# Optimization experiments

Measured on AMD Instinct MI355X. Metric: run time of the kernel, lower is better.

Reference implementation:

```python
import jax, jax.numpy as jnp
import numpy as np
from jax import lax

B, T, F = 8, 512, 128          # batch, mel time, mel freq
DM, DS, DC, EXP, NL = 384, 16, 4, 2, 12
DI = EXP * DM                   # 768 inner width
DTR = (DM + 15) // 16           # 24, mamba_ssm dt_rank='auto'
PT = PF = 16
L = (T // PT) * (F // PF)       # 256 patches
NC = 4


def setup_inputs() -> dict:
    key = jax.random.key(0)
    ks = iter(jax.random.split(key, 24))
    def n(shape, s=0.02):
        return jax.random.normal(next(ks), shape, jnp.float32) * s
    return {
        "x": jax.random.normal(next(ks), (B, T, F), jnp.float32),
        "patch_w": n((DM, PT, PF)),
        "patch_b": jnp.zeros((DM,), jnp.float32),
        "pos_embed": n((1, L, DM)),
        "ln_g": jnp.ones((NL, DM), jnp.float32),
        "ln_b": jnp.zeros((NL, DM), jnp.float32),
        "in_proj_w": n((NL, 2 * DI, DM)),
        "conv_w": n((NL, DI, DC), 0.1),
        "conv_b": jnp.zeros((NL, DI), jnp.float32),
        "x_proj_w": n((NL, DTR + 2 * DS, DI)),
        "dt_proj_w": n((NL, DI, DTR), 0.1),
        "dt_proj_b": n((NL, DI), 0.1),
        "A_log": jnp.tile(jnp.log(jnp.arange(1, DS + 1, dtype=jnp.float32))[None, None, :], (NL, DI, 1)),
        "Dskip": jnp.ones((NL, DI), jnp.float32),
        "out_proj_w": n((NL, DM, DI)),
        "fn_g": jnp.ones((DM,), jnp.float32),
        "fn_b": jnp.zeros((DM,), jnp.float32),
        "head_w": n((NC, DM)),
        "head_b": jnp.zeros((NC,), jnp.float32),
    }


def _layernorm(x, g, b):
    m = x.mean(-1, keepdims=True)
    v = jnp.var(x, axis=-1, keepdims=True)
    return (x - m) * lax.rsqrt(v + 1e-5) * g + b


def _silu(v):
    return v * jax.nn.sigmoid(v)


def _mamba_block(x, p):
    # x: [B, L, DM]; residual Mamba block (pre-LN, dropout=identity in eval)
    ln_g, ln_b, Wi, cw, cb, Wx, Wdt, bdt, A_log, Dsk, Wo = p
    res = x
    h = _layernorm(x, ln_g, ln_b)
    xz = jnp.einsum('bld,ed->ble', h, Wi)          # [B,L,2*DI]
    u, z = jnp.split(xz, 2, axis=-1)
    # causal depthwise conv1d, kernel DC (small, unrolled)
    up = jnp.pad(u, ((0, 0), (DC - 1, 0), (0, 0)))
    u = sum(up[:, k:k + L, :] * cw[:, k] for k in range(DC)) + cb
    u = _silu(u)
    proj = jnp.einsum('bld,ed->ble', u, Wx)        # [B,L,DTR+2*DS]
    dt, Bm, Cm = jnp.split(proj, [DTR, DTR + DS], axis=-1)
    delta = jax.nn.softplus(jnp.einsum('blr,dr->bld', dt, Wdt) + bdt)  # [B,L,DI]
    A = -jnp.exp(A_log)                            # [DI, DS]
    dA = jnp.exp(delta[..., None] * A)             # [B,L,DI,DS]
    dBu = (delta * u)[..., None] * Bm[:, :, None, :]

    def step(hst, inp):
        dA_t, dBu_t, C_t = inp
        hst = dA_t * hst + dBu_t                   # [B,DI,DS]
        return hst, jnp.einsum('bdn,bn->bd', hst, C_t)

    h0 = jnp.zeros((x.shape[0], DI, DS), x.dtype)
    _, ys = lax.scan(step, h0, (dA.swapaxes(0, 1), dBu.swapaxes(0, 1), Cm.swapaxes(0, 1)))
    y = ys.swapaxes(0, 1) + u * Dsk                # [B,L,DI]
    y = y * _silu(z)
    return res + jnp.einsum('bld,ed->ble', y, Wo)


def reference(x, patch_w, patch_b, pos_embed, ln_g, ln_b, in_proj_w, conv_w, conv_b,
              x_proj_w, dt_proj_w, dt_proj_b, A_log, Dskip, out_proj_w,
              fn_g, fn_b, head_w, head_b):
    Bn = x.shape[0]
    # patch embed = non-overlapping 16x16 conv == blocked reshape + einsum
    patches = x.reshape(Bn, T // PT, PT, F // PF, PF)
    tok = jnp.einsum('bhpwq,dpq->bhwd', patches, patch_w) + patch_b
    tok = tok.reshape(Bn, L, DM) + pos_embed

    def layer(carry, p):
        return _mamba_block(carry, p), None

    tok, _ = lax.scan(layer, tok, (ln_g, ln_b, in_proj_w, conv_w, conv_b,
                                   x_proj_w, dt_proj_w, dt_proj_b, A_log, Dskip, out_proj_w))
    tok = _layernorm(tok, fn_g, fn_b)
    pooled = tok.mean(axis=1)
    return pooled @ head_w.T + head_b
```

## Files before the change

kernel.cpp:

```cpp
#include <hip/hip_runtime.h>
#include <math.h>

namespace {

constexpr int kB   = 8;
constexpr int kL   = 256;
constexpr int kTok = 2048;
constexpr int kDM  = 384;
constexpr int kDI  = 768;
constexpr int kDS  = 16;
constexpr int kDTR = 24;
constexpr int kPROJ = 56;
constexpr int kNL  = 12;

constexpr int kWIN  = 2 * kDI * kDM;
constexpr int kWOUT = kDM * kDI;
constexpr int kWX   = kPROJ * kDI;
constexpr int kWTOT = kWIN + kWOUT + kWX;

typedef float f32x4 __attribute__((ext_vector_type(4)));
typedef short short8 __attribute__((ext_vector_type(8)));

__device__ __forceinline__ float softplus_f(float x) {
  return (x > 20.f) ? x : log1pf(__expf(x));
}
__device__ __forceinline__ float silu_f(float x) {
  return x / (1.f + __expf(-x));
}
__device__ __forceinline__ unsigned short f2bf(float f) {
  union { float f; unsigned u; } v; v.f = f;
  unsigned r = v.u + 0x7FFFu + ((v.u >> 16) & 1u);
  return (unsigned short)(r >> 16);
}

__global__ __launch_bounds__(256) void patch_gemm_k(
    const float* __restrict__ x, const float* __restrict__ Bw,
    const float* __restrict__ bias, const float* __restrict__ pos,
    float* __restrict__ C) {
  __shared__ float As[16][68];
  __shared__ float Bs[16][68];
  int tid = threadIdx.x;
  int bm = blockIdx.y * 64;
  int bn = blockIdx.x * 64;
  int lr = tid >> 2;
  int lk = (tid & 3) << 2;
  int tm = (tid >> 4) << 2;
  int tn = (tid & 15) << 2;
  float acc[4][4] = {};
  for (int k0 = 0; k0 < 256; k0 += 16) {
    {
      int token = bm + lr;
      int b = token >> 8, l = token & 255;
      int h = l >> 3, w = l & 7;
      int p = k0 >> 4;
      const float* ap = x + ((size_t)(b * 512) + h * 16 + p) * 128 + w * 16 + lk;
      float4 av = *(const float4*)ap;
      As[lk + 0][lr] = av.x; As[lk + 1][lr] = av.y;
      As[lk + 2][lr] = av.z; As[lk + 3][lr] = av.w;
    }
    {
      const float* bp = Bw + (size_t)(bn + lr) * 256 + k0 + lk;
      float4 bv = *(const float4*)bp;
      Bs[lk + 0][lr] = bv.x; Bs[lk + 1][lr] = bv.y;
      Bs[lk + 2][lr] = bv.z; Bs[lk + 3][lr] = bv.w;
    }
    __syncthreads();
    #pragma unroll
    for (int k = 0; k < 16; ++k) {
      float4 a = *(const float4*)&As[k][tm];
      float4 b = *(const float4*)&Bs[k][tn];
      float av[4] = {a.x, a.y, a.z, a.w};
      float bv[4] = {b.x, b.y, b.z, b.w};
      #pragma unroll
      for (int i = 0; i < 4; ++i)
        #pragma unroll
        for (int j = 0; j < 4; ++j)
          acc[i][j] = fmaf(av[i], bv[j], acc[i][j]);
    }
    __syncthreads();
  }
  #pragma unroll
  for (int i = 0; i < 4; ++i) {
    int row = bm + tm + i;
    #pragma unroll
    for (int j = 0; j < 4; ++j) {
      int col = bn + tn + j;
      C[(size_t)row * kDM + col] =
          acc[i][j] + bias[col] + pos[(size_t)(row & 255) * kDM + col];
    }
  }
}

template <bool BF16OUT>
__global__ __launch_bounds__(384) void ln_k(
    const float* __restrict__ in, void* __restrict__ outv,
    const float* __restrict__ g, const float* __restrict__ bb,
    float* __restrict__ proj_zero) {
  int t = blockIdx.x, d = threadIdx.x;
  if (proj_zero && d < kPROJ) proj_zero[(size_t)t * kPROJ + d] = 0.f;
  float v = in[(size_t)t * kDM + d];
  float s = v, s2 = v * v;
  #pragma unroll
  for (int m = 32; m >= 1; m >>= 1) {
    s  += __shfl_xor(s, m);
    s2 += __shfl_xor(s2, m);
  }
  __shared__ float ps[6], ps2[6];
  if ((d & 63) == 0) { ps[d >> 6] = s; ps2[d >> 6] = s2; }
  __syncthreads();
  float S = 0.f, S2 = 0.f;
  #pragma unroll
  for (int i = 0; i < 6; ++i) { S += ps[i]; S2 += ps2[i]; }
  float mean = S * (1.f / 384.f);
  float var  = S2 * (1.f / 384.f) - mean * mean;
  float r = rsqrtf(var + 1e-5f);
  float o = (v - mean) * r * g[d] + bb[d];
  if (BF16OUT) ((unsigned short*)outv)[(size_t)t * kDM + d] = f2bf(o);
  else ((float*)outv)[(size_t)t * kDM + d] = o;
}

__global__ __launch_bounds__(256) void convert_all_k(
    const float* __restrict__ w_in, const float* __restrict__ w_out,
    const float* __restrict__ w_x, unsigned short* __restrict__ dst) {
  int layer = blockIdx.y;
  int i4 = (blockIdx.x * 256 + threadIdx.x) * 4;
  if (i4 >= kWTOT) return;
  const float* src;
  int off;
  if (i4 < kWIN) { src = w_in + (size_t)layer * kWIN; off = i4; }
  else if (i4 < kWIN + kWOUT) { src = w_out + (size_t)layer * kWOUT; off = i4 - kWIN; }
  else { src = w_x + (size_t)layer * kWX; off = i4 - kWIN - kWOUT; }
  float4 v = *(const float4*)(src + off);
  unsigned short o[4] = {f2bf(v.x), f2bf(v.y), f2bf(v.z), f2bf(v.w)};
  *(uint2*)(dst + (size_t)layer * kWTOT + i4) = *(const uint2*)o;
}

template <int BN, int EPIL>
__global__ __launch_bounds__(256) void bgemm_k(
    const unsigned short* __restrict__ A, int lda,
    const unsigned short* __restrict__ B, int ldb,
    float* __restrict__ C, int ldc, int N, int Kc) {
  __shared__ __align__(16) unsigned short As[4][128][8];
  __shared__ __align__(16) unsigned short Bs[4][BN][8];
  int tid = threadIdx.x;
  int bm = blockIdx.y * 128;
  int bn = blockIdx.x * BN;
  int k_begin = blockIdx.z * Kc;
  int wave = tid >> 6, lane = tid & 63;
  int lm = lane & 15, lq = lane >> 4;
  int wm, wn;
  if (BN == 128) { wm = (wave >> 1) * 64; wn = (wave & 1) * 64; }
  else           { wm = wave * 32;        wn = 0; }
  constexpr int MT = (BN == 128) ? 4 : 2;
  f32x4 acc[MT][4] = {};

  for (int kt = 0; kt < Kc; kt += 32) {
    int k0 = k_begin + kt;
    int ar0 = tid & 127, aq0 = tid >> 7;
    int aq1 = aq0 + 2;
    uint4 a0 = *(const uint4*)(A + (size_t)(bm + ar0) * lda + k0 + aq0 * 8);
    uint4 a1 = *(const uint4*)(A + (size_t)(bm + ar0) * lda + k0 + aq1 * 8);
    uint4 b0, b1;
    int br0, bq0, br1 = 0, bq1 = 0;
    if (BN == 128) {
      br0 = tid & 127; bq0 = tid >> 7; br1 = br0; bq1 = bq0 + 2;
      b0 = *(const uint4*)(B + (size_t)(bn + br0) * ldb + k0 + bq0 * 8);
      b1 = *(const uint4*)(B + (size_t)(bn + br1) * ldb + k0 + bq1 * 8);
    } else {
      br0 = tid & 63; bq0 = tid >> 6;
      if (bn + br0 < N)
        b0 = *(const uint4*)(B + (size_t)(bn + br0) * ldb + k0 + bq0 * 8);
      else
        b0 = make_uint4(0u, 0u, 0u, 0u);
    }
    __syncthreads();
    *(uint4*)&As[aq0][ar0][0] = a0;
    *(uint4*)&As[aq1][ar0][0] = a1;
    *(uint4*)&Bs[bq0][br0][0] = b0;
    if (BN == 128) *(uint4*)&Bs[bq1][br1][0] = b1;
    __syncthreads();

    short8 bfrag[4];
    #pragma unroll
    for (int ni = 0; ni < 4; ++ni)
      bfrag[ni] = *(const short8*)&Bs[lq][wn + ni * 16 + lm][0];
    #pragma unroll
    for (int mi = 0; mi < MT; ++mi) {
      short8 afrag = *(const short8*)&As[lq][wm + mi * 16 + lm][0];
      #pragma unroll
      for (int ni = 0; ni < 4; ++ni)
        acc[mi][ni] = __builtin_amdgcn_mfma_f32_16x16x32_bf16(
            afrag, bfrag[ni], acc[mi][ni], 0, 0, 0);
    }
  }

  #pragma unroll
  for (int mi = 0; mi < MT; ++mi) {
    #pragma unroll
    for (int ni = 0; ni < 4; ++ni) {
      int grow = bm + wm + mi * 16 + lq * 4;
      int gcol = bn + wn + ni * 16 + lm;
      float* cp = C + (size_t)grow * ldc + gcol;
      #pragma unroll
      for (int r = 0; r < 4; ++r) {
        float v = acc[mi][ni][r];
        if (EPIL == 0) {
          cp[(size_t)r * ldc] = v;
        } else {
          if (gcol < N) atomicAdd(cp + (size_t)r * ldc, v);
        }
      }
    }
  }
}

__global__ __launch_bounds__(256) void conv_tr_k(
    const float* __restrict__ xz, const float* __restrict__ cw,
    const float* __restrict__ cb, float* __restrict__ uT,
    float* __restrict__ sgT, unsigned short* __restrict__ u_bf) {
  int b = blockIdx.y;
  int l0 = blockIdx.x * 16;
  int tid = threadIdx.x;
  #pragma unroll
  for (int ch = 0; ch < 3; ++ch) {
    int d = ch * 256 + tid;
    float w0 = cw[d * 4], w1 = cw[d * 4 + 1], w2 = cw[d * 4 + 2], w3 = cw[d * 4 + 3];
    float bias = cb[d];
    float v[19];
    #pragma unroll
    for (int j = 0; j < 19; ++j) {
      int l = l0 - 3 + j;
      v[j] = (l >= 0) ? xz[(size_t)(b * kL + l) * (2 * kDI) + d] : 0.f;
    }
    float* up = uT + ((size_t)b * kDI + d) * kL + l0;
    float* sp = sgT + ((size_t)b * kDI + d) * kL + l0;
    #pragma unroll
    for (int i = 0; i < 16; ++i) {
      float acc = bias;
      acc = fmaf(v[i], w0, acc);
      acc = fmaf(v[i + 1], w1, acc);
      acc = fmaf(v[i + 2], w2, acc);
      acc = fmaf(v[i + 3], w3, acc);
      float o = silu_f(acc);
      up[i] = o;
      u_bf[(size_t)(b * kL + l0 + i) * kDI + d] = f2bf(o);
      float zv = xz[(size_t)(b * kL + l0 + i) * (2 * kDI) + kDI + d];
      sp[i] = silu_f(zv);
    }
  }
}

__global__ __launch_bounds__(256) void scan2_k(
    const float* __restrict__ proj, const float* __restrict__ uT,
    const float* __restrict__ sgT, const float* __restrict__ dtw,
    const float* __restrict__ dtb, const float* __restrict__ A_log,
    const float* __restrict__ Dsk, float* __restrict__ yT) {
  int d = blockIdx.x;
  int b = blockIdx.y;
  int tid = threadIdx.x;
  int c = tid >> 4;
  int n = tid & 15;
  __shared__ float sd[256], su[256], sg[256], sy[256];
  __shared__ float sh_h[16][17], sh_a[16][17];
  __shared__ float swdt[24];
  size_t rbase = ((size_t)b * kDI + d) * kL;
  su[tid] = uT[rbase + tid];
  sg[tid] = sgT[rbase + tid];
  if (tid < kDTR) swdt[tid] = dtw[(size_t)d * kDTR + tid];
  float bdt = dtb[d];
  float Aval = -__expf(A_log[d * kDS + n]);
  __syncthreads();
  {
    const float* pr = proj + (size_t)(b * kL + tid) * kPROJ;
    float acc = bdt;
    #pragma unroll
    for (int r4 = 0; r4 < 6; ++r4) {
      float4 pv = *(const float4*)(pr + r4 * 4);
      acc = fmaf(pv.x, swdt[r4 * 4 + 0], acc);
      acc = fmaf(pv.y, swdt[r4 * 4 + 1], acc);
      acc = fmaf(pv.z, swdt[r4 * 4 + 2], acc);
      acc = fmaf(pv.w, swdt[r4 * 4 + 3], acc);
    }
    sd[tid] = softplus_f(acc);
  }
  __syncthreads();

  float h = 0.f, ca = 1.f;
  float h_reg[16], ca_reg[16], cv[16];
  const float* pp = proj + (size_t)(b * kL + c * 16) * kPROJ;
  #pragma unroll
  for (int i = 0; i < 16; ++i) {
    int l = c * 16 + i;
    float dl = sd[l], uv = su[l];
    float Bv = pp[i * kPROJ + kDTR + n];
    cv[i] = pp[i * kPROJ + kDTR + kDS + n];
    float a = __expf(dl * Aval);
    h = fmaf(a, h, (dl * uv) * Bv);
    ca *= a;
    h_reg[i] = h;
    ca_reg[i] = ca;
  }
  sh_h[c][n] = h;
  sh_a[c][n] = ca;
  __syncthreads();

  float h0 = 0.f;
  for (int j = 0; j < c; ++j) h0 = fmaf(sh_a[j][n], h0, sh_h[j][n]);

  float Dv = Dsk[d];
  #pragma unroll
  for (int i = 0; i < 16; ++i) {
    int l = c * 16 + i;
    float yv = fmaf(ca_reg[i], h0, h_reg[i]) * cv[i];
    yv += __shfl_xor(yv, 1);
    yv += __shfl_xor(yv, 2);
    yv += __shfl_xor(yv, 4);
    yv += __shfl_xor(yv, 8);
    if (n == 0) sy[l] = (yv + su[l] * Dv) * sg[l];
  }
  __syncthreads();
  yT[rbase + tid] = sy[tid];
}

__global__ __launch_bounds__(256) void transpose_bf_k(
    const float* __restrict__ yT, unsigned short* __restrict__ ybf) {
  int b = blockIdx.z;
  int db = blockIdx.y;
  int lb = blockIdx.x;
  __shared__ float tile[64][65];
  int tid = threadIdx.x;
  int lx = tid & 63, dq = tid >> 6;
  const float* src = yT + ((size_t)b * kDI + db * 64) * kL + lb * 64;
  #pragma unroll
  for (int i = 0; i < 16; ++i) {
    int d = dq * 16 + i;
    tile[d][lx] = src[(size_t)d * kL + lx];
  }
  __syncthreads();
  int ly = tid >> 2, dx0 = (tid & 3) * 16;
  unsigned short tmp[16];
  #pragma unroll
  for (int i = 0; i < 16; ++i) tmp[i] = f2bf(tile[dx0 + i][ly]);
  unsigned short* dst =
      ybf + (size_t)(b * kL + lb * 64 + ly) * kDI + db * 64 + dx0;
  *(uint4*)dst = *(const uint4*)tmp;
  *(uint4*)(dst + 8) = *(const uint4*)(tmp + 8);
}

__global__ __launch_bounds__(384) void pool_k(
    const float* __restrict__ h, float* __restrict__ pooled) {
  int b = blockIdx.x, d = threadIdx.x;
  float acc = 0.f;
  for (int l = 0; l < kL; ++l) acc += h[(size_t)(b * kL + l) * kDM + d];
  pooled[b * kDM + d] = acc * (1.f / 256.f);
}

__global__ __launch_bounds__(64) void head_k(
    const float* __restrict__ pooled, const float* __restrict__ hw,
    const float* __restrict__ hb, float* __restrict__ out) {
  int b = blockIdx.x >> 2, c = blockIdx.x & 3;
  int lane = threadIdx.x;
  float acc = 0.f;
  for (int dd = lane; dd < kDM; dd += 64)
    acc = fmaf(pooled[b * kDM + dd], hw[c * kDM + dd], acc);
  #pragma unroll
  for (int m = 32; m >= 1; m >>= 1) acc += __shfl_xor(acc, m);
  if (lane == 0) out[b * 4 + c] = acc + hb[c];
}

}

extern "C" void kernel_launch(void* const* d_in, const int* in_sizes, int n_in,
                              void* d_out, int out_size, void* d_ws, size_t ws_size,
                              hipStream_t stream) {
  (void)in_sizes; (void)n_in; (void)out_size; (void)ws_size;
  const float* x        = (const float*)d_in[0];
  const float* patch_w  = (const float*)d_in[1];
  const float* patch_b  = (const float*)d_in[2];
  const float* pos      = (const float*)d_in[3];
  const float* ln_g     = (const float*)d_in[4];
  const float* ln_b     = (const float*)d_in[5];
  const float* in_w     = (const float*)d_in[6];
  const float* conv_w   = (const float*)d_in[7];
  const float* conv_b   = (const float*)d_in[8];
  const float* xproj_w  = (const float*)d_in[9];
  const float* dtproj_w = (const float*)d_in[10];
  const float* dtproj_b = (const float*)d_in[11];
  const float* A_log    = (const float*)d_in[12];
  const float* Dskip    = (const float*)d_in[13];
  const float* out_w    = (const float*)d_in[14];
  const float* fn_g     = (const float*)d_in[15];
  const float* fn_b     = (const float*)d_in[16];
  const float* head_w   = (const float*)d_in[17];
  const float* head_b   = (const float*)d_in[18];
  float* out = (float*)d_out;

  float* ws = (float*)d_ws;
  float* tok    = ws; ws += kTok * kDM;
  float* xz     = ws; ws += kTok * 2 * kDI;
  float* uT     = ws; ws += kTok * kDI;
  float* sgT    = ws; ws += kTok * kDI;
  float* proj   = ws; ws += kTok * kPROJ;
  float* yT     = ws; ws += kTok * kDI;
  float* pooled = ws; ws += kB * kDM;
  unsigned short* h_bf = (unsigned short*)ws; ws += kTok * kDM / 2;
  unsigned short* y_bf = (unsigned short*)ws; ws += kTok * kDI / 2;
  unsigned short* u_bf = (unsigned short*)ws; ws += kTok * kDI / 2;
  unsigned short* w_bf = (unsigned short*)ws; ws += (size_t)kNL * kWTOT / 2;
  float* lnout = yT;

  convert_all_k<<<dim3(kWTOT / 4 / 256, kNL), 256, 0, stream>>>(
      in_w, out_w, xproj_w, w_bf);

  patch_gemm_k<<<dim3(6, 32), 256, 0, stream>>>(x, patch_w, patch_b, pos, tok);

  for (int layer = 0; layer < kNL; ++layer) {
    const unsigned short* wl = w_bf + (size_t)layer * kWTOT;
    ln_k<true><<<kTok, kDM, 0, stream>>>(tok, h_bf, ln_g + layer * kDM,
                                         ln_b + layer * kDM, proj);
    bgemm_k<128, 0><<<dim3(12, 16, 1), 256, 0, stream>>>(
        h_bf, kDM, wl, kDM, xz, 2 * kDI, 2 * kDI, kDM);
    conv_tr_k<<<dim3(16, kB), 256, 0, stream>>>(
        xz, conv_w + layer * kDI * 4, conv_b + layer * kDI, uT, sgT, u_bf);
    bgemm_k<64, 1><<<dim3(1, 16, 6), 256, 0, stream>>>(
        u_bf, kDI, wl + kWIN + kWOUT, kDI, proj, kPROJ, kPROJ, kDI / 6);
    scan2_k<<<dim3(kDI, kB), 256, 0, stream>>>(
        proj, uT, sgT, dtproj_w + (size_t)layer * kDI * kDTR,
        dtproj_b + layer * kDI, A_log + (size_t)layer * kDI * kDS,
        Dskip + layer * kDI, yT);
    transpose_bf_k<<<dim3(4, 12, kB), 256, 0, stream>>>(yT, y_bf);
    bgemm_k<128, 1><<<dim3(3, 16, 2), 256, 0, stream>>>(
        y_bf, kDI, wl + kWIN, kDI, tok, kDM, kDM, kDI / 2);
  }

  ln_k<false><<<kTok, kDM, 0, stream>>>(tok, lnout, fn_g, fn_b, nullptr);
  pool_k<<<kB, kDM, 0, stream>>>(lnout, pooled);
  head_k<<<kB * 4, 64, 0, stream>>>(pooled, head_w, head_b, out);
}
```

Measured before the change: 1.364 ms.

## Transpose proj layout for coalesced scan reads, emit bf16 scan output, raise split-K

The x_proj GEMM epilogue now atomically adds into a transposed [B, PROJ, L] buffer, so the scan kernel reads B/C coefficients as contiguous float4 vectors and dt inputs with coalesced loads instead of strided per-token rows. The scan writes its y output directly as bf16, which halves the intermediate traffic, and the transpose kernel only shuffles bits. Split-K factors for the x_proj and out_proj GEMMs are doubled to expose more blocks, at the cost of more atomic traffic. The scan output is rounded to bf16 one step earlier, but the same rounding already happened in the transpose.

```diff
diff --git a/kernel.cpp b/kernel.cpp
--- a/kernel.cpp
+++ b/kernel.cpp
@@ -198,16 +198,19 @@
   for (int mi = 0; mi < MT; ++mi) {
     #pragma unroll
     for (int ni = 0; ni < 4; ++ni) {
-      int grow = bm + wm + mi * 16 + lq * 4;
+      int grow0 = bm + wm + mi * 16 + lq * 4;
       int gcol = bn + wn + ni * 16 + lm;
-      float* cp = C + (size_t)grow * ldc + gcol;
       #pragma unroll
       for (int r = 0; r < 4; ++r) {
         float v = acc[mi][ni][r];
+        int grow = grow0 + r;
         if (EPIL == 0) {
-          cp[(size_t)r * ldc] = v;
+          C[(size_t)grow * ldc + gcol] = v;
+        } else if (EPIL == 1) {
+          if (gcol < N) atomicAdd(&C[(size_t)grow * ldc + gcol], v);
         } else {
-          if (gcol < N) atomicAdd(cp + (size_t)r * ldc, v);
+          if (gcol < N)
+            atomicAdd(&C[((size_t)(grow >> 8) * kPROJ + gcol) * kL + (grow & 255)], v);
         }
       }
     }
@@ -250,17 +253,18 @@
   }
 }
 
-__global__ __launch_bounds__(256) void scan2_k(
-    const float* __restrict__ proj, const float* __restrict__ uT,
+__global__ __launch_bounds__(256) void scan3_k(
+    const float* __restrict__ projT, const float* __restrict__ uT,
     const float* __restrict__ sgT, const float* __restrict__ dtw,
     const float* __restrict__ dtb, const float* __restrict__ A_log,
-    const float* __restrict__ Dsk, float* __restrict__ yT) {
+    const float* __restrict__ Dsk, unsigned short* __restrict__ yT) {
   int d = blockIdx.x;
   int b = blockIdx.y;
   int tid = threadIdx.x;
   int c = tid >> 4;
   int n = tid & 15;
-  __shared__ float sd[256], su[256], sg[256], sy[256];
+  __shared__ float sd[256], su[256], sg[256];
+  __shared__ unsigned short sy[256];
   __shared__ float sh_h[16][17], sh_a[16][17];
   __shared__ float swdt[24];
   size_t rbase = ((size_t)b * kDI + d) * kL;
@@ -269,33 +273,43 @@
   if (tid < kDTR) swdt[tid] = dtw[(size_t)d * kDTR + tid];
   float bdt = dtb[d];
   float Aval = -__expf(A_log[d * kDS + n]);
-  __syncthreads();
+  const float* pb = projT + (size_t)b * kPROJ * kL;
+  float4 Bv4[4], Cv4[4];
   {
-    const float* pr = proj + (size_t)(b * kL + tid) * kPROJ;
+    const float* prB = pb + (size_t)(24 + n) * kL + c * 16;
+    const float* prC = pb + (size_t)(40 + n) * kL + c * 16;
+    #pragma unroll
+    for (int q = 0; q < 4; ++q) {
+      Bv4[q] = ((const float4*)prB)[q];
+      Cv4[q] = ((const float4*)prC)[q];
+    }
+  }
+  float B_[16], C_[16];
+  #pragma unroll
+  for (int q = 0; q < 4; ++q) {
+    B_[q * 4 + 0] = Bv4[q].x; B_[q * 4 + 1] = Bv4[q].y;
+    B_[q * 4 + 2] = Bv4[q].z; B_[q * 4 + 3] = Bv4[q].w;
+    C_[q * 4 + 0] = Cv4[q].x; C_[q * 4 + 1] = Cv4[q].y;
+    C_[q * 4 + 2] = Cv4[q].z; C_[q * 4 + 3] = Cv4[q].w;
+  }
+  __syncthreads();
+  {
     float acc = bdt;
     #pragma unroll
-    for (int r4 = 0; r4 < 6; ++r4) {
-      float4 pv = *(const float4*)(pr + r4 * 4);
-      acc = fmaf(pv.x, swdt[r4 * 4 + 0], acc);
-      acc = fmaf(pv.y, swdt[r4 * 4 + 1], acc);
-      acc = fmaf(pv.z, swdt[r4 * 4 + 2], acc);
-      acc = fmaf(pv.w, swdt[r4 * 4 + 3], acc);
-    }
+    for (int r = 0; r < kDTR; ++r)
+      acc = fmaf(pb[(size_t)r * kL + tid], swdt[r], acc);
     sd[tid] = softplus_f(acc);
   }
   __syncthreads();
 
   float h = 0.f, ca = 1.f;
-  float h_reg[16], ca_reg[16], cv[16];
-  const float* pp = proj + (size_t)(b * kL + c * 16) * kPROJ;
+  float h_reg[16], ca_reg[16];
   #pragma unroll
   for (int i = 0; i < 16; ++i) {
     int l = c * 16 + i;
-    float dl = sd[l], uv = su[l];
-    float Bv = pp[i * kPROJ + kDTR + n];
-    cv[i] = pp[i * kPROJ + kDTR + kDS + n];
+    float dl = sd[l];
     float a = __expf(dl * Aval);
-    h = fmaf(a, h, (dl * uv) * Bv);
+    h = fmaf(a, h, (dl * su[l]) * B_[i]);
     ca *= a;
     h_reg[i] = h;
     ca_reg[i] = ca;
@@ -311,36 +325,38 @@
   #pragma unroll
   for (int i = 0; i < 16; ++i) {
     int l = c * 16 + i;
-    float yv = fmaf(ca_reg[i], h0, h_reg[i]) * cv[i];
+    float yv = fmaf(ca_reg[i], h0, h_reg[i]) * C_[i];
     yv += __shfl_xor(yv, 1);
     yv += __shfl_xor(yv, 2);
     yv += __shfl_xor(yv, 4);
     yv += __shfl_xor(yv, 8);
-    if (n == 0) sy[l] = (yv + su[l] * Dv) * sg[l];
+    if (n == 0) sy[l] = f2bf((yv + su[l] * Dv) * sg[l]);
   }
   __syncthreads();
   yT[rbase + tid] = sy[tid];
 }
 
 __global__ __launch_bounds__(256) void transpose_bf_k(
-    const float* __restrict__ yT, unsigned short* __restrict__ ybf) {
+    const unsigned short* __restrict__ yT, unsigned short* __restrict__ ybf) {
   int b = blockIdx.z;
   int db = blockIdx.y;
   int lb = blockIdx.x;
   __shared__ float tile[64][65];
   int tid = threadIdx.x;
   int lx = tid & 63, dq = tid >> 6;
-  const float* src = yT + ((size_t)b * kDI + db * 64) * kL + lb * 64;
+  const unsigned short* src = yT + ((size_t)b * kDI + db * 64) * kL + lb * 64;
   #pragma unroll
   for (int i = 0; i < 16; ++i) {
-    int d = dq * 16 + i;
-    tile[d][lx] = src[(size_t)d * kL + lx];
+    int dd = dq * 16 + i;
+    unsigned ui = (unsigned)src[(size_t)dd * kL + lx] << 16;
+    tile[dd][lx] = __uint_as_float(ui);
   }
   __syncthreads();
   int ly = tid >> 2, dx0 = (tid & 3) * 16;
   unsigned short tmp[16];
   #pragma unroll
-  for (int i = 0; i < 16; ++i) tmp[i] = f2bf(tile[dx0 + i][ly]);
+  for (int i = 0; i < 16; ++i)
+    tmp[i] = (unsigned short)(__float_as_uint(tile[dx0 + i][ly]) >> 16);
   unsigned short* dst =
       ybf + (size_t)(b * kL + lb * 64 + ly) * kDI + db * 64 + dx0;
   *(uint4*)dst = *(const uint4*)tmp;
@@ -400,14 +416,14 @@
   float* xz     = ws; ws += kTok * 2 * kDI;
   float* uT     = ws; ws += kTok * kDI;
   float* sgT    = ws; ws += kTok * kDI;
-  float* proj   = ws; ws += kTok * kPROJ;
-  float* yT     = ws; ws += kTok * kDI;
+  float* projT  = ws; ws += kTok * kPROJ;
   float* pooled = ws; ws += kB * kDM;
-  unsigned short* h_bf = (unsigned short*)ws; ws += kTok * kDM / 2;
-  unsigned short* y_bf = (unsigned short*)ws; ws += kTok * kDI / 2;
-  unsigned short* u_bf = (unsigned short*)ws; ws += kTok * kDI / 2;
-  unsigned short* w_bf = (unsigned short*)ws; ws += (size_t)kNL * kWTOT / 2;
-  float* lnout = yT;
+  unsigned short* yT_bf = (unsigned short*)ws; ws += kTok * kDI / 2;
+  unsigned short* h_bf  = (unsigned short*)ws; ws += kTok * kDM / 2;
+  unsigned short* y_bf  = (unsigned short*)ws; ws += kTok * kDI / 2;
+  unsigned short* u_bf  = (unsigned short*)ws; ws += kTok * kDI / 2;
+  unsigned short* w_bf  = (unsigned short*)ws; ws += (size_t)kNL * kWTOT / 2;
+  float* lnout = xz;
 
   convert_all_k<<<dim3(kWTOT / 4 / 256, kNL), 256, 0, stream>>>(
       in_w, out_w, xproj_w, w_bf);
@@ -417,20 +433,20 @@
   for (int layer = 0; layer < kNL; ++layer) {
     const unsigned short* wl = w_bf + (size_t)layer * kWTOT;
     ln_k<true><<<kTok, kDM, 0, stream>>>(tok, h_bf, ln_g + layer * kDM,
-                                         ln_b + layer * kDM, proj);
+                                         ln_b + layer * kDM, projT);
     bgemm_k<128, 0><<<dim3(12, 16, 1), 256, 0, stream>>>(
         h_bf, kDM, wl, kDM, xz, 2 * kDI, 2 * kDI, kDM);
     conv_tr_k<<<dim3(16, kB), 256, 0, stream>>>(
         xz, conv_w + layer * kDI * 4, conv_b + layer * kDI, uT, sgT, u_bf);
-    bgemm_k<64, 1><<<dim3(1, 16, 6), 256, 0, stream>>>(
-        u_bf, kDI, wl + kWIN + kWOUT, kDI, proj, kPROJ, kPROJ, kDI / 6);
-    scan2_k<<<dim3(kDI, kB), 256, 0, stream>>>(
-        proj, uT, sgT, dtproj_w + (size_t)layer * kDI * kDTR,
+    bgemm_k<64, 2><<<dim3(1, 16, 12), 256, 0, stream>>>(
+        u_bf, kDI, wl + kWIN + kWOUT, kDI, projT, 0, kPROJ, kDI / 12);
+    scan3_k<<<dim3(kDI, kB), 256, 0, stream>>>(
+        projT, uT, sgT, dtproj_w + (size_t)layer * kDI * kDTR,
         dtproj_b + layer * kDI, A_log + (size_t)layer * kDI * kDS,
-        Dskip + layer * kDI, yT);
-    transpose_bf_k<<<dim3(4, 12, kB), 256, 0, stream>>>(yT, y_bf);
-    bgemm_k<128, 1><<<dim3(3, 16, 2), 256, 0, stream>>>(
-        y_bf, kDI, wl + kWIN, kDI, tok, kDM, kDM, kDI / 2);
+        Dskip + layer * kDI, yT_bf);
+    transpose_bf_k<<<dim3(4, 12, kB), 256, 0, stream>>>(yT_bf, y_bf);
+    bgemm_k<128, 1><<<dim3(3, 16, 4), 256, 0, stream>>>(
+        y_bf, kDI, wl + kWIN, kDI, tok, kDM, kDM, kDI / 4);
   }
 
   ln_k<false><<<kTok, kDM, 0, stream>>>(tok, lnout, fn_g, fn_b, nullptr);
```

New measurement: 1.528 ms. 1.12x slower.

## Fuse layernorm into in-proj GEMM and batch scan over 8 channels writing bf16

Applied to the files above, without the earlier changes.

LayerNorm is now computed inside the input-projection GEMM: per-row statistics go to shared memory, and the A tile is normalized and converted to bf16 on the fly, so the separate LN kernel and its bf16 activation buffer are gone. The selective-scan kernel now handles 8 inner channels per block, loading B/C once into shared memory, and writes the bf16 row-major output directly. This removes the fp32 yT buffer and the transpose kernel. Zeroing of the proj accumulator moves into the conv kernel. The trade-offs are fewer scan blocks (768 instead of 6144), less parallelism, and redundant normalization work across the 12 column blocks.

```diff
diff --git a/kernel.cpp b/kernel.cpp
--- a/kernel.cpp
+++ b/kernel.cpp
@@ -91,13 +91,10 @@
   }
 }
 
-template <bool BF16OUT>
 __global__ __launch_bounds__(384) void ln_k(
-    const float* __restrict__ in, void* __restrict__ outv,
-    const float* __restrict__ g, const float* __restrict__ bb,
-    float* __restrict__ proj_zero) {
+    const float* __restrict__ in, float* __restrict__ outv,
+    const float* __restrict__ g, const float* __restrict__ bb) {
   int t = blockIdx.x, d = threadIdx.x;
-  if (proj_zero && d < kPROJ) proj_zero[(size_t)t * kPROJ + d] = 0.f;
   float v = in[(size_t)t * kDM + d];
   float s = v, s2 = v * v;
   #pragma unroll
@@ -114,9 +111,7 @@
   float mean = S * (1.f / 384.f);
   float var  = S2 * (1.f / 384.f) - mean * mean;
   float r = rsqrtf(var + 1e-5f);
-  float o = (v - mean) * r * g[d] + bb[d];
-  if (BF16OUT) ((unsigned short*)outv)[(size_t)t * kDM + d] = f2bf(o);
-  else ((float*)outv)[(size_t)t * kDM + d] = o;
+  outv[(size_t)t * kDM + d] = (v - mean) * r * g[d] + bb[d];
 }
 
 __global__ __launch_bounds__(256) void convert_all_k(
@@ -133,6 +128,93 @@
   float4 v = *(const float4*)(src + off);
   unsigned short o[4] = {f2bf(v.x), f2bf(v.y), f2bf(v.z), f2bf(v.w)};
   *(uint2*)(dst + (size_t)layer * kWTOT + i4) = *(const uint2*)o;
+}
+
+__global__ __launch_bounds__(256) void inproj_ln_k(
+    const float* __restrict__ tok, const unsigned short* __restrict__ Bw,
+    const float* __restrict__ g, const float* __restrict__ bb,
+    float* __restrict__ C) {
+  __shared__ __align__(16) unsigned short As[4][128][8];
+  __shared__ __align__(16) unsigned short Bs[4][128][8];
+  __shared__ float smean[128], srstd[128];
+  __shared__ float sg_[kDM], sb_[kDM];
+  int tid = threadIdx.x;
+  int bm = blockIdx.y * 128;
+  int bn = blockIdx.x * 128;
+  for (int i = tid; i < kDM; i += 256) { sg_[i] = g[i]; sb_[i] = bb[i]; }
+  {
+    int r = tid >> 1, half = tid & 1;
+    const float* rp = tok + (size_t)(bm + r) * kDM + half * 192;
+    float s = 0.f, s2 = 0.f;
+    #pragma unroll
+    for (int q = 0; q < 48; ++q) {
+      float4 v = ((const float4*)rp)[q];
+      s  += v.x + v.y + v.z + v.w;
+      s2 += v.x * v.x + v.y * v.y + v.z * v.z + v.w * v.w;
+    }
+    s  += __shfl_xor(s, 1);
+    s2 += __shfl_xor(s2, 1);
+    if (half == 0) {
+      float mean = s * (1.f / 384.f);
+      float var  = s2 * (1.f / 384.f) - mean * mean;
+      smean[r] = mean;
+      srstd[r] = rsqrtf(var + 1e-5f);
+    }
+  }
+  __syncthreads();
+  int wave = tid >> 6, lane = tid & 63;
+  int lm = lane & 15, lq = lane >> 4;
+  int wm = (wave >> 1) * 64, wn = (wave & 1) * 64;
+  f32x4 acc[4][4] = {};
+  for (int k0 = 0; k0 < kDM; k0 += 32) {
+    int ar0 = tid & 127, aq0 = tid >> 7;
+    unsigned short av[2][8];
+    float mean = smean[ar0], rstd = srstd[ar0];
+    #pragma unroll
+    for (int gq = 0; gq < 2; ++gq) {
+      int kq = aq0 + gq * 2;
+      const float* ap = tok + (size_t)(bm + ar0) * kDM + k0 + kq * 8;
+      float4 v0 = ((const float4*)ap)[0];
+      float4 v1 = ((const float4*)ap)[1];
+      float vv[8] = {v0.x, v0.y, v0.z, v0.w, v1.x, v1.y, v1.z, v1.w};
+      #pragma unroll
+      for (int j = 0; j < 8; ++j) {
+        int k = k0 + kq * 8 + j;
+        av[gq][j] = f2bf((vv[j] - mean) * rstd * sg_[k] + sb_[k]);
+      }
+    }
+    uint4 b0 = *(const uint4*)(Bw + (size_t)(bn + ar0) * kDM + k0 + aq0 * 8);
+    uint4 b1 = *(const uint4*)(Bw + (size_t)(bn + ar0) * kDM + k0 + (aq0 + 2) * 8);
+    __syncthreads();
+    *(uint4*)&As[aq0][ar0][0]     = *(const uint4*)av[0];
+    *(uint4*)&As[aq0 + 2][ar0][0] = *(const uint4*)av[1];
+    *(uint4*)&Bs[aq0][ar0][0]     = b0;
+    *(uint4*)&Bs[aq0 + 2][ar0][0] = b1;
+    __syncthreads();
+    short8 bfrag[4];
+    #pragma unroll
+    for (int ni = 0; ni < 4; ++ni)
+      bfrag[ni] = *(const short8*)&Bs[lq][wn + ni * 16 + lm][0];
+    #pragma unroll
+    for (int mi = 0; mi < 4; ++mi) {
+      short8 afrag = *(const short8*)&As[lq][wm + mi * 16 + lm][0];
+      #pragma unroll
+      for (int ni = 0; ni < 4; ++ni)
+        acc[mi][ni] = __builtin_amdgcn_mfma_f32_16x16x32_bf16(
+            afrag, bfrag[ni], acc[mi][ni], 0, 0, 0);
+    }
+  }
+  #pragma unroll
+  for (int mi = 0; mi < 4; ++mi) {
+    #pragma unroll
+    for (int ni = 0; ni < 4; ++ni) {
+      int grow0 = bm + wm + mi * 16 + lq * 4;
+      int gcol = bn + wn + ni * 16 + lm;
+      #pragma unroll
+      for (int r = 0; r < 4; ++r)
+        C[(size_t)(grow0 + r) * (2 * kDI) + gcol] = acc[mi][ni][r];
+    }
+  }
 }
 
 template <int BN, int EPIL>
@@ -198,16 +280,16 @@
   for (int mi = 0; mi < MT; ++mi) {
     #pragma unroll
     for (int ni = 0; ni < 4; ++ni) {
-      int grow = bm + wm + mi * 16 + lq * 4;
+      int grow0 = bm + wm + mi * 16 + lq * 4;
       int gcol = bn + wn + ni * 16 + lm;
-      float* cp = C + (size_t)grow * ldc + gcol;
       #pragma unroll
       for (int r = 0; r < 4; ++r) {
         float v = acc[mi][ni][r];
+        int grow = grow0 + r;
         if (EPIL == 0) {
-          cp[(size_t)r * ldc] = v;
+          C[(size_t)grow * ldc + gcol] = v;
         } else {
-          if (gcol < N) atomicAdd(cp + (size_t)r * ldc, v);
+          if (gcol < N) atomicAdd(&C[(size_t)grow * ldc + gcol], v);
         }
       }
     }
@@ -217,10 +299,15 @@
 __global__ __launch_bounds__(256) void conv_tr_k(
     const float* __restrict__ xz, const float* __restrict__ cw,
     const float* __restrict__ cb, float* __restrict__ uT,
-    float* __restrict__ sgT, unsigned short* __restrict__ u_bf) {
+    float* __restrict__ sgT, unsigned short* __restrict__ u_bf,
+    float* __restrict__ proj_zero) {
   int b = blockIdx.y;
   int l0 = blockIdx.x * 16;
   int tid = threadIdx.x;
+  {
+    int gid = (blockIdx.y * 16 + blockIdx.x) * 256 + tid;
+    for (int i = gid; i < kTok * kPROJ; i += 16 * kB * 256) proj_zero[i] = 0.f;
+  }
   #pragma unroll
   for (int ch = 0; ch < 3; ++ch) {
     int d = ch * 256 + tid;
@@ -250,101 +337,91 @@
   }
 }
 
-__global__ __launch_bounds__(256) void scan2_k(
+__global__ __launch_bounds__(256) void scan8_k(
     const float* __restrict__ proj, const float* __restrict__ uT,
     const float* __restrict__ sgT, const float* __restrict__ dtw,
     const float* __restrict__ dtb, const float* __restrict__ A_log,
-    const float* __restrict__ Dsk, float* __restrict__ yT) {
-  int d = blockIdx.x;
+    const float* __restrict__ Dsk, unsigned short* __restrict__ y_bf) {
+  int d0 = blockIdx.x * 8;
   int b = blockIdx.y;
   int tid = threadIdx.x;
-  int c = tid >> 4;
-  int n = tid & 15;
-  __shared__ float sd[256], su[256], sg[256], sy[256];
+  int c = tid >> 4, n = tid & 15;
+  __shared__ float sBC[256][33];
+  __shared__ float sdall[8][256];
+  __shared__ float su[256], sg[256];
   __shared__ float sh_h[16][17], sh_a[16][17];
-  __shared__ float swdt[24];
-  size_t rbase = ((size_t)b * kDI + d) * kL;
-  su[tid] = uT[rbase + tid];
-  sg[tid] = sgT[rbase + tid];
-  if (tid < kDTR) swdt[tid] = dtw[(size_t)d * kDTR + tid];
-  float bdt = dtb[d];
-  float Aval = -__expf(A_log[d * kDS + n]);
+  __shared__ float swdt[8][24];
+  __shared__ float sAv[8][16];
+  __shared__ float sbdt[8], sDv[8];
+  __shared__ unsigned short sy[256][8];
+
+  {
+    const float* pr = proj + ((size_t)(b * kL) + tid) * kPROJ + 24;
+    #pragma unroll
+    for (int q = 0; q < 8; ++q)
+      *(float4*)&sBC[tid][q * 4] = ((const float4*)pr)[q];
+  }
+  if (tid < 192) swdt[tid / 24][tid % 24] =
+      dtw[(size_t)(d0 + tid / 24) * kDTR + (tid % 24)];
+  if (tid < 128) sAv[tid >> 4][tid & 15] =
+      -__expf(A_log[(size_t)(d0 + (tid >> 4)) * kDS + (tid & 15)]);
+  if (tid < 8) { sbdt[tid] = dtb[d0 + tid]; sDv[tid] = Dsk[d0 + tid]; }
   __syncthreads();
+
   {
-    const float* pr = proj + (size_t)(b * kL + tid) * kPROJ;
-    float acc = bdt;
-    #pragma unroll
-    for (int r4 = 0; r4 < 6; ++r4) {
-      float4 pv = *(const float4*)(pr + r4 * 4);
-      acc = fmaf(pv.x, swdt[r4 * 4 + 0], acc);
-      acc = fmaf(pv.y, swdt[r4 * 4 + 1], acc);
-      acc = fmaf(pv.z, swdt[r4 * 4 + 2], acc);
-      acc = fmaf(pv.w, swdt[r4 * 4 + 3], acc);
-    }
-    sd[tid] = softplus_f(acc);
+    const float* pr = proj + ((size_t)(b * kL) + tid) * kPROJ;
+    float p[24];
+    #pragma unroll
+    for (int q = 0; q < 6; ++q) {
+      float4 v = ((const float4*)pr)[q];
+      p[q * 4] = v.x; p[q * 4 + 1] = v.y; p[q * 4 + 2] = v.z; p[q * 4 + 3] = v.w;
+    }
+    #pragma unroll
+    for (int dd = 0; dd < 8; ++dd) {
+      float acc = sbdt[dd];
+      #pragma unroll
+      for (int r = 0; r < 24; ++r) acc = fmaf(p[r], swdt[dd][r], acc);
+      sdall[dd][tid] = softplus_f(acc);
+    }
   }
   __syncthreads();
 
-  float h = 0.f, ca = 1.f;
-  float h_reg[16], ca_reg[16], cv[16];
-  const float* pp = proj + (size_t)(b * kL + c * 16) * kPROJ;
-  #pragma unroll
-  for (int i = 0; i < 16; ++i) {
-    int l = c * 16 + i;
-    float dl = sd[l], uv = su[l];
-    float Bv = pp[i * kPROJ + kDTR + n];
-    cv[i] = pp[i * kPROJ + kDTR + kDS + n];
-    float a = __expf(dl * Aval);
-    h = fmaf(a, h, (dl * uv) * Bv);
-    ca *= a;
-    h_reg[i] = h;
-    ca_reg[i] = ca;
-  }
-  sh_h[c][n] = h;
-  sh_a[c][n] = ca;
-  __syncthreads();
-
-  float h0 = 0.f;
-  for (int j = 0; j < c; ++j) h0 = fmaf(sh_a[j][n], h0, sh_h[j][n]);
-
-  float Dv = Dsk[d];
-  #pragma unroll
-  for (int i = 0; i < 16; ++i) {
-    int l = c * 16 + i;
-    float yv = fmaf(ca_reg[i], h0, h_reg[i]) * cv[i];
-    yv += __shfl_xor(yv, 1);
-    yv += __shfl_xor(yv, 2);
-    yv += __shfl_xor(yv, 4);
-    yv += __shfl_xor(yv, 8);
-    if (n == 0) sy[l] = (yv + su[l] * Dv) * sg[l];
-  }
-  __syncthreads();
-  yT[rbase + tid] = sy[tid];
-}
-
-__global__ __launch_bounds__(256) void transpose_bf_k(
-    const float* __restrict__ yT, unsigned short* __restrict__ ybf) {
-  int b = blockIdx.z;
-  int db = blockIdx.y;
-  int lb = blockIdx.x;
-  __shared__ float tile[64][65];
-  int tid = threadIdx.x;
-  int lx = tid & 63, dq = tid >> 6;
-  const float* src = yT + ((size_t)b * kDI + db * 64) * kL + lb * 64;
-  #pragma unroll
-  for (int i = 0; i < 16; ++i) {
-    int d = dq * 16 + i;
-    tile[d][lx] = src[(size_t)d * kL + lx];
-  }
-  __syncthreads();
-  int ly = tid >> 2, dx0 = (tid & 3) * 16;
-  unsigned short tmp[16];
-  #pragma unroll
-  for (int i = 0; i < 16; ++i) tmp[i] = f2bf(tile[dx0 + i][ly]);
-  unsigned short* dst =
-      ybf + (size_t)(b * kL + lb * 64 + ly) * kDI + db * 64 + dx0;
-  *(uint4*)dst = *(const uint4*)tmp;
-  *(uint4*)(dst + 8) = *(const uint4*)(tmp + 8);
+  for (int dd = 0; dd < 8; ++dd) {
+    int d = d0 + dd;
+    size_t rbase = ((size_t)b * kDI + d) * kL;
+    su[tid] = uT[rbase + tid];
+    sg[tid] = sgT[rbase + tid];
+    float Av = sAv[dd][n];
+    __syncthreads();
+    float h = 0.f, ca = 1.f;
+    float h_reg[16], ca_reg[16];
+    #pragma unroll
+    for (int i = 0; i < 16; ++i) {
+      int l = c * 16 + i;
+      float dl = sdall[dd][l];
+      float a = __expf(dl * Av);
+      h = fmaf(a, h, (dl * su[l]) * sBC[l][n]);
+      ca *= a;
+      h_reg[i] = h; ca_reg[i] = ca;
+    }
+    sh_h[c][n] = h; sh_a[c][n] = ca;
+    __syncthreads();
+    float h0 = 0.f;
+    for (int j = 0; j < c; ++j) h0 = fmaf(sh_a[j][n], h0, sh_h[j][n]);
+    float Dv = sDv[dd];
+    #pragma unroll
+    for (int i = 0; i < 16; ++i) {
+      int l = c * 16 + i;
+      float yv = fmaf(ca_reg[i], h0, h_reg[i]) * sBC[l][16 + n];
+      yv += __shfl_xor(yv, 1);
+      yv += __shfl_xor(yv, 2);
+      yv += __shfl_xor(yv, 4);
+      yv += __shfl_xor(yv, 8);
+      if (n == 0) sy[l][dd] = f2bf((yv + su[l] * Dv) * sg[l]);
+    }
+    __syncthreads();
+  }
+  *(uint4*)(y_bf + ((size_t)(b * kL) + tid) * kDI + d0) = *(const uint4*)&sy[tid][0];
 }
 
 __global__ __launch_bounds__(384) void pool_k(
@@ -401,13 +478,11 @@
   float* uT     = ws; ws += kTok * kDI;
   float* sgT    = ws; ws += kTok * kDI;
   float* proj   = ws; ws += kTok * kPROJ;
-  float* yT     = ws; ws += kTok * kDI;
   float* pooled = ws; ws += kB * kDM;
-  unsigned short* h_bf = (unsigned short*)ws; ws += kTok * kDM / 2;
   unsigned short* y_bf = (unsigned short*)ws; ws += kTok * kDI / 2;
   unsigned short* u_bf = (unsigned short*)ws; ws += kTok * kDI / 2;
   unsigned short* w_bf = (unsigned short*)ws; ws += (size_t)kNL * kWTOT / 2;
-  float* lnout = yT;
+  float* lnout = xz;
 
   convert_all_k<<<dim3(kWTOT / 4 / 256, kNL), 256, 0, stream>>>(
       in_w, out_w, xproj_w, w_bf);
@@ -416,24 +491,21 @@
 
   for (int layer = 0; layer < kNL; ++layer) {
     const unsigned short* wl = w_bf + (size_t)layer * kWTOT;
-    ln_k<true><<<kTok, kDM, 0, stream>>>(tok, h_bf, ln_g + layer * kDM,
-                                         ln_b + layer * kDM, proj);
-    bgemm_k<128, 0><<<dim3(12, 16, 1), 256, 0, stream>>>(
-        h_bf, kDM, wl, kDM, xz, 2 * kDI, 2 * kDI, kDM);
+    inproj_ln_k<<<dim3(12, 16), 256, 0, stream>>>(
+        tok, wl, ln_g + layer * kDM, ln_b + layer * kDM, xz);
     conv_tr_k<<<dim3(16, kB), 256, 0, stream>>>(
-        xz, conv_w + layer * kDI * 4, conv_b + layer * kDI, uT, sgT, u_bf);
+        xz, conv_w + layer * kDI * 4, conv_b + layer * kDI, uT, sgT, u_bf, proj);
     bgemm_k<64, 1><<<dim3(1, 16, 6), 256, 0, stream>>>(
         u_bf, kDI, wl + kWIN + kWOUT, kDI, proj, kPROJ, kPROJ, kDI / 6);
-    scan2_k<<<dim3(kDI, kB), 256, 0, stream>>>(
+    scan8_k<<<dim3(kDI / 8, kB), 256, 0, stream>>>(
         proj, uT, sgT, dtproj_w + (size_t)layer * kDI * kDTR,
         dtproj_b + layer * kDI, A_log + (size_t)layer * kDI * kDS,
-        Dskip + layer * kDI, yT);
-    transpose_bf_k<<<dim3(4, 12, kB), 256, 0, stream>>>(yT, y_bf);
+        Dskip + layer * kDI, y_bf);
     bgemm_k<128, 1><<<dim3(3, 16, 2), 256, 0, stream>>>(
         y_bf, kDI, wl + kWIN, kDI, tok, kDM, kDM, kDI / 2);
   }
 
-  ln_k<false><<<kTok, kDM, 0, stream>>>(tok, lnout, fn_g, fn_b, nullptr);
+  ln_k<<<kTok, kDM, 0, stream>>>(tok, lnout, fn_g, fn_b);
   pool_k<<<kB, kDM, 0, stream>>>(lnout, pooled);
   head_k<<<kB * 4, 64, 0, stream>>>(pooled, head_w, head_b, out);
 }
```

Measured after the change: 1.559 ms. +14.3%, slower.
